# Kernel tuning notes

Measured on AMD Instinct MI355X. Metric: run time of the kernel, lower is better.

## Reference

```python
import math
import functools
import jax, jax.numpy as jnp
import numpy as np


def setup_inputs() -> dict:
    key = jax.random.key(0)
    ks = jax.random.split(key, 7)
    header = jax.random.normal(ks[0], (4, 4), dtype=jnp.float32) + 4.0 * jnp.eye(4, dtype=jnp.float32)  # well-conditioned
    vol_affine = jax.random.normal(ks[1], (4, 4), dtype=jnp.float32)
    cr = jax.random.normal(ks[2], (3,), dtype=jnp.float32)          # rotation center (mean of self.crs)
    normvec = jax.random.normal(ks[3], (3,), dtype=jnp.float32)     # mean plane normal (pre sign-align/mean)
    translation = jax.random.normal(ks[4], (3,), dtype=jnp.float32)
    angle = jax.random.normal(ks[5], (3,), dtype=jnp.float32) * 10.0  # degrees
    scaling = jax.random.normal(ks[6], (2,), dtype=jnp.float32)
    return {"header": header, "vol_affine": vol_affine, "cr": cr, "normvec": normvec,
            "translation": translation, "angle": angle, "scaling": scaling}


def _compute_affine_matrix(cr, normvec, translation, angle, scaling):
    I4 = jnp.eye(4, dtype=jnp.float32)
    nv = normvec / jnp.linalg.norm(normvec)
    norm_xy = jnp.linalg.norm(nv[:2])

    # T1 / T1inv: translate rotation center to / from origin
    T1 = I4.at[:3, 3].set(-cr)
    T1inv = I4.at[:3, 3].set(cr)

    # T2 / T2inv: rotate normal's xy-projection onto x-axis (identity if norm_xy == 0)
    zero_xy = norm_xy == 0
    safe = jnp.where(zero_xy, 1.0, norm_xy)
    a = jnp.where(zero_xy, 1.0, nv[0] / safe)
    b = jnp.where(zero_xy, 0.0, nv[1] / safe)
    T2 = I4.at[0, 0].set(a).at[0, 1].set(b).at[1, 0].set(-b).at[1, 1].set(a)
    T2inv = I4.at[0, 0].set(a).at[0, 1].set(-b).at[1, 0].set(b).at[1, 1].set(a)

    # T3 / T3inv: rotate normal onto z-axis
    T3 = I4.at[0, 0].set(nv[2]).at[0, 2].set(-norm_xy).at[2, 0].set(norm_xy).at[2, 2].set(nv[2])
    T3inv = I4.at[0, 0].set(nv[2]).at[0, 2].set(norm_xy).at[2, 0].set(-norm_xy).at[2, 2].set(nv[2])

    # T4a: anisotropic scaling (XY shared, Z separate), exp-parameterized
    sxy = jnp.exp(scaling[0] / 100.0)
    sz = jnp.exp(scaling[1] / 100.0)
    T4a = I4.at[0, 0].set(sxy).at[1, 1].set(sxy).at[2, 2].set(sz)

    # T4b1/2/3: rotations about x, y, z (angles in degrees)
    ang = angle / 180.0 * math.pi
    c, s = jnp.cos(ang), jnp.sin(ang)
    T4b1 = I4.at[1, 1].set(c[0]).at[1, 2].set(-s[0]).at[2, 1].set(s[0]).at[2, 2].set(c[0])
    T4b2 = I4.at[0, 0].set(c[1]).at[0, 2].set(s[1]).at[2, 0].set(-s[1]).at[2, 2].set(c[1])
    T4b3 = I4.at[0, 0].set(c[2]).at[0, 1].set(-s[2]).at[1, 0].set(s[2]).at[1, 1].set(c[2])

    Ttrans = I4.at[:3, 3].set(translation)

    mats = [Ttrans, T1inv, T2inv, T3inv, T4b3, T4b2, T4b1, T4a, T3, T2, T1]
    return functools.reduce(jnp.matmul, mats)


def reference(header, vol_affine, cr, normvec, translation, angle, scaling):
    ndims = 3
    T = _compute_affine_matrix(cr, normvec, translation, angle, scaling)
    new_header = T @ header                                  # [4,4]
    affine_full = jnp.linalg.inv(new_header) @ vol_affine    # [4,4]
    affine = affine_full[:ndims][None]                       # [1,3,4] (unsqueeze then [:ndims] slices batch dim of size 1)
    return affine, new_header
```

## Files before the change

kernel.cpp:

```cpp
#include <hip/hip_runtime.h>
#include <math.h>


__device__ inline void matmul4(const float* A, const float* B, float* C) {
    for (int i = 0; i < 4; ++i)
        for (int j = 0; j < 4; ++j) {
            float s = 0.0f;
            for (int k = 0; k < 4; ++k) s = fmaf(A[i*4+k], B[k*4+j], s);
            C[i*4+j] = s;
        }
}

__device__ inline void eye4(float* M) {
    for (int i = 0; i < 16; ++i) M[i] = 0.0f;
    M[0] = M[5] = M[10] = M[15] = 1.0f;
}

__global__ void affine_kernel(const float* __restrict__ header,
                              const float* __restrict__ vol_affine,
                              const float* __restrict__ cr,
                              const float* __restrict__ normvec,
                              const float* __restrict__ translation,
                              const float* __restrict__ angle,
                              const float* __restrict__ scaling,
                              float* __restrict__ out) {
    if (threadIdx.x != 0 || blockIdx.x != 0) return;

    const float PI = 3.14159265358979323846f;

    float n0 = normvec[0], n1 = normvec[1], n2 = normvec[2];
    float nn = sqrtf(fmaf(n0, n0, fmaf(n1, n1, n2 * n2)));
    float nv0 = n0 / nn, nv1 = n1 / nn, nv2 = n2 / nn;
    float norm_xy = sqrtf(fmaf(nv0, nv0, nv1 * nv1));

    bool zero_xy = (norm_xy == 0.0f);
    float safe = zero_xy ? 1.0f : norm_xy;
    float a = zero_xy ? 1.0f : nv0 / safe;
    float b = zero_xy ? 0.0f : nv1 / safe;

    float T1[16], T1inv[16], T2[16], T2inv[16], T3[16], T3inv[16];
    float T4a[16], Ttrans[16];

    eye4(T1);    T1[3]    = -cr[0]; T1[7]    = -cr[1]; T1[11]    = -cr[2];
    eye4(T1inv); T1inv[3] =  cr[0]; T1inv[7] =  cr[1]; T1inv[11] =  cr[2];

    eye4(T2);    T2[0] = a;    T2[1] = b;     T2[4] = -b;    T2[5] = a;
    eye4(T2inv); T2inv[0] = a; T2inv[1] = -b; T2inv[4] = b;  T2inv[5] = a;

    eye4(T3);    T3[0] = nv2;    T3[2] = -norm_xy;    T3[8] = norm_xy;     T3[10] = nv2;
    eye4(T3inv); T3inv[0] = nv2; T3inv[2] = norm_xy;  T3inv[8] = -norm_xy; T3inv[10] = nv2;

    float sxy = __expf(scaling[0] * 0.01f);
    float sz  = __expf(scaling[1] * 0.01f);
    eye4(T4a); T4a[0] = sxy; T4a[5] = sxy; T4a[10] = sz;

    float a0 = angle[0] * (PI / 180.0f);
    float a1 = angle[1] * (PI / 180.0f);
    float a2 = angle[2] * (PI / 180.0f);
    float s0, c0, s1, c1, s2, c2;
    __sincosf(a0, &s0, &c0);
    __sincosf(a1, &s1, &c1);
    __sincosf(a2, &s2, &c2);
    float T4b1_[16], T4b2_[16], T4b3_[16];
    eye4(T4b1_); T4b1_[5] = c0; T4b1_[6] = -s0; T4b1_[9] = s0;  T4b1_[10] = c0;
    eye4(T4b2_); T4b2_[0] = c1; T4b2_[2] = s1;  T4b2_[8] = -s1; T4b2_[10] = c1;
    eye4(T4b3_); T4b3_[0] = c2; T4b3_[1] = -s2; T4b3_[4] = s2;  T4b3_[5] = c2;

    eye4(Ttrans);
    Ttrans[3]  = translation[0];
    Ttrans[7]  = translation[1];
    Ttrans[11] = translation[2];

    float acc[16], tmp[16];
    matmul4(Ttrans, T1inv, acc);
    matmul4(acc, T2inv, tmp);
    matmul4(tmp, T3inv, acc);
    matmul4(acc, T4b3_, tmp);
    matmul4(tmp, T4b2_, acc);
    matmul4(acc, T4b1_, tmp);
    matmul4(tmp, T4a, acc);
    matmul4(acc, T3, tmp);
    matmul4(tmp, T2, acc);
    matmul4(acc, T1, tmp);

    float H[16];
    for (int i = 0; i < 16; ++i) H[i] = header[i];
    float NH[16];
    matmul4(tmp, H, NH);

    float M[16], Inv[16];
    for (int i = 0; i < 16; ++i) M[i] = NH[i];
    eye4(Inv);
    for (int col = 0; col < 4; ++col) {
        int piv = col;
        float best = fabsf(M[col * 4 + col]);
        for (int r = col + 1; r < 4; ++r) {
            float v = fabsf(M[r * 4 + col]);
            if (v > best) { best = v; piv = r; }
        }
        if (piv != col) {
            for (int j = 0; j < 4; ++j) {
                float t = M[col * 4 + j]; M[col * 4 + j] = M[piv * 4 + j]; M[piv * 4 + j] = t;
                t = Inv[col * 4 + j]; Inv[col * 4 + j] = Inv[piv * 4 + j]; Inv[piv * 4 + j] = t;
            }
        }
        float invd = 1.0f / M[col * 4 + col];
        for (int j = 0; j < 4; ++j) { M[col * 4 + j] *= invd; Inv[col * 4 + j] *= invd; }
        for (int r = 0; r < 4; ++r) {
            if (r == col) continue;
            float f = M[r * 4 + col];
            if (f != 0.0f) {
                for (int j = 0; j < 4; ++j) {
                    M[r * 4 + j]   = fmaf(-f, M[col * 4 + j],   M[r * 4 + j]);
                    Inv[r * 4 + j] = fmaf(-f, Inv[col * 4 + j], Inv[r * 4 + j]);
                }
            }
        }
    }

    float VA[16];
    for (int i = 0; i < 16; ++i) VA[i] = vol_affine[i];
    float AF[16];
    matmul4(Inv, VA, AF);

    for (int i = 0; i < 12; ++i) out[i]      = AF[i];
    for (int i = 0; i < 16; ++i) out[12 + i] = NH[i];
}

extern "C" void kernel_launch(void* const* d_in, const int* in_sizes, int n_in,
                              void* d_out, int out_size, void* d_ws, size_t ws_size,
                              hipStream_t stream) {
    const float* header      = (const float*)d_in[0];
    const float* vol_affine  = (const float*)d_in[1];
    const float* cr          = (const float*)d_in[2];
    const float* normvec     = (const float*)d_in[3];
    const float* translation = (const float*)d_in[4];
    const float* angle       = (const float*)d_in[5];
    const float* scaling     = (const float*)d_in[6];
    float* out = (float*)d_out;

    affine_kernel<<<1, 64, 0, stream>>>(header, vol_affine, cr, normvec,
                                        translation, angle, scaling, out);
}
```

Before: 9.719 us.

## Compose affine as 3x3 rotation plus translation and use closed-form 4x4 inverse

Replaces the chain of eleven 4x4 homogeneous matmuls with six 3x3 products, merging scaling into the x-rotation and folding the translate/center terms into one translation vector. Replaces pivoted Gauss-Jordan inversion with a cofactor (2x2 sub-determinant) closed-form inverse, and computes only the needed rows of the final products. This cuts serial single-thread arithmetic and branching. The closed-form inverse drops pivoting, which can change numerical accuracy for ill-conditioned headers.

```diff
diff --git a/kernel.cpp b/kernel.cpp
--- a/kernel.cpp
+++ b/kernel.cpp
@@ -2,18 +2,14 @@
 #include <math.h>
 
 
-__device__ inline void matmul4(const float* A, const float* B, float* C) {
-    for (int i = 0; i < 4; ++i)
-        for (int j = 0; j < 4; ++j) {
-            float s = 0.0f;
-            for (int k = 0; k < 4; ++k) s = fmaf(A[i*4+k], B[k*4+j], s);
-            C[i*4+j] = s;
+__device__ inline void mm3(const float* A, const float* B, float* C) {
+    for (int i = 0; i < 3; ++i)
+        for (int j = 0; j < 3; ++j) {
+            float s = A[i*3+0] * B[0*3+j];
+            s = fmaf(A[i*3+1], B[1*3+j], s);
+            s = fmaf(A[i*3+2], B[2*3+j], s);
+            C[i*3+j] = s;
         }
-}
-
-__device__ inline void eye4(float* M) {
-    for (int i = 0; i < 16; ++i) M[i] = 0.0f;
-    M[0] = M[5] = M[10] = M[15] = 1.0f;
 }
 
 __global__ void affine_kernel(const float* __restrict__ header,
@@ -31,28 +27,15 @@
     float n0 = normvec[0], n1 = normvec[1], n2 = normvec[2];
     float nn = sqrtf(fmaf(n0, n0, fmaf(n1, n1, n2 * n2)));
     float nv0 = n0 / nn, nv1 = n1 / nn, nv2 = n2 / nn;
-    float norm_xy = sqrtf(fmaf(nv0, nv0, nv1 * nv1));
+    float nxy = sqrtf(fmaf(nv0, nv0, nv1 * nv1));
 
-    bool zero_xy = (norm_xy == 0.0f);
-    float safe = zero_xy ? 1.0f : norm_xy;
+    bool zero_xy = (nxy == 0.0f);
+    float safe = zero_xy ? 1.0f : nxy;
     float a = zero_xy ? 1.0f : nv0 / safe;
     float b = zero_xy ? 0.0f : nv1 / safe;
 
-    float T1[16], T1inv[16], T2[16], T2inv[16], T3[16], T3inv[16];
-    float T4a[16], Ttrans[16];
-
-    eye4(T1);    T1[3]    = -cr[0]; T1[7]    = -cr[1]; T1[11]    = -cr[2];
-    eye4(T1inv); T1inv[3] =  cr[0]; T1inv[7] =  cr[1]; T1inv[11] =  cr[2];
-
-    eye4(T2);    T2[0] = a;    T2[1] = b;     T2[4] = -b;    T2[5] = a;
-    eye4(T2inv); T2inv[0] = a; T2inv[1] = -b; T2inv[4] = b;  T2inv[5] = a;
-
-    eye4(T3);    T3[0] = nv2;    T3[2] = -norm_xy;    T3[8] = norm_xy;     T3[10] = nv2;
-    eye4(T3inv); T3inv[0] = nv2; T3inv[2] = norm_xy;  T3inv[8] = -norm_xy; T3inv[10] = nv2;
-
     float sxy = __expf(scaling[0] * 0.01f);
     float sz  = __expf(scaling[1] * 0.01f);
-    eye4(T4a); T4a[0] = sxy; T4a[5] = sxy; T4a[10] = sz;
 
     float a0 = angle[0] * (PI / 180.0f);
     float a1 = angle[1] * (PI / 180.0f);
@@ -61,69 +44,89 @@
     __sincosf(a0, &s0, &c0);
     __sincosf(a1, &s1, &c1);
     __sincosf(a2, &s2, &c2);
-    float T4b1_[16], T4b2_[16], T4b3_[16];
-    eye4(T4b1_); T4b1_[5] = c0; T4b1_[6] = -s0; T4b1_[9] = s0;  T4b1_[10] = c0;
-    eye4(T4b2_); T4b2_[0] = c1; T4b2_[2] = s1;  T4b2_[8] = -s1; T4b2_[10] = c1;
-    eye4(T4b3_); T4b3_[0] = c2; T4b3_[1] = -s2; T4b3_[4] = s2;  T4b3_[5] = c2;
 
-    eye4(Ttrans);
-    Ttrans[3]  = translation[0];
-    Ttrans[7]  = translation[1];
-    Ttrans[11] = translation[2];
+    float T23[9]    = { a,  b, 0.0f,  -b,  a, 0.0f,  0.0f, 0.0f, 1.0f };
+    float T2inv3[9] = { a, -b, 0.0f,   b,  a, 0.0f,  0.0f, 0.0f, 1.0f };
+    float T33[9]    = { nv2, 0.0f, -nxy,  0.0f, 1.0f, 0.0f,  nxy, 0.0f, nv2 };
+    float T3inv3[9] = { nv2, 0.0f,  nxy,  0.0f, 1.0f, 0.0f, -nxy, 0.0f, nv2 };
+    float Rz[9]     = { c2, -s2, 0.0f,  s2, c2, 0.0f,  0.0f, 0.0f, 1.0f };
+    float Ry[9]     = { c1, 0.0f, s1,   0.0f, 1.0f, 0.0f,  -s1, 0.0f, c1 };
+    float RxS[9]    = { sxy, 0.0f, 0.0f,
+                        0.0f, sxy * c0, -sz * s0,
+                        0.0f, sxy * s0,  sz * c0 };
 
-    float acc[16], tmp[16];
-    matmul4(Ttrans, T1inv, acc);
-    matmul4(acc, T2inv, tmp);
-    matmul4(tmp, T3inv, acc);
-    matmul4(acc, T4b3_, tmp);
-    matmul4(tmp, T4b2_, acc);
-    matmul4(acc, T4b1_, tmp);
-    matmul4(tmp, T4a, acc);
-    matmul4(acc, T3, tmp);
-    matmul4(tmp, T2, acc);
-    matmul4(acc, T1, tmp);
+    float A1[9], A2[9], M[9];
+    mm3(T2inv3, T3inv3, A1);
+    mm3(A1, Rz, A2);
+    mm3(A2, Ry, A1);
+    mm3(A1, RxS, A2);
+    mm3(A2, T33, A1);
+    mm3(A1, T23, M);
+
+    float cr0 = cr[0], cr1 = cr[1], cr2 = cr[2];
+    float t0 = translation[0] + cr0 - (fmaf(M[0], cr0, fmaf(M[1], cr1, M[2] * cr2)));
+    float t1 = translation[1] + cr1 - (fmaf(M[3], cr0, fmaf(M[4], cr1, M[5] * cr2)));
+    float t2 = translation[2] + cr2 - (fmaf(M[6], cr0, fmaf(M[7], cr1, M[8] * cr2)));
+    float t[3] = { t0, t1, t2 };
 
     float H[16];
     for (int i = 0; i < 16; ++i) H[i] = header[i];
     float NH[16];
-    matmul4(tmp, H, NH);
+    for (int i = 0; i < 3; ++i)
+        for (int j = 0; j < 4; ++j) {
+            float s = fmaf(M[i*3+0], H[0*4+j],
+                      fmaf(M[i*3+1], H[1*4+j],
+                      fmaf(M[i*3+2], H[2*4+j],
+                           t[i] * H[3*4+j])));
+            NH[i*4+j] = s;
+        }
+    for (int j = 0; j < 4; ++j) NH[12 + j] = H[12 + j];
 
-    float M[16], Inv[16];
-    for (int i = 0; i < 16; ++i) M[i] = NH[i];
-    eye4(Inv);
-    for (int col = 0; col < 4; ++col) {
-        int piv = col;
-        float best = fabsf(M[col * 4 + col]);
-        for (int r = col + 1; r < 4; ++r) {
-            float v = fabsf(M[r * 4 + col]);
-            if (v > best) { best = v; piv = r; }
-        }
-        if (piv != col) {
-            for (int j = 0; j < 4; ++j) {
-                float t = M[col * 4 + j]; M[col * 4 + j] = M[piv * 4 + j]; M[piv * 4 + j] = t;
-                t = Inv[col * 4 + j]; Inv[col * 4 + j] = Inv[piv * 4 + j]; Inv[piv * 4 + j] = t;
-            }
-        }
-        float invd = 1.0f / M[col * 4 + col];
-        for (int j = 0; j < 4; ++j) { M[col * 4 + j] *= invd; Inv[col * 4 + j] *= invd; }
-        for (int r = 0; r < 4; ++r) {
-            if (r == col) continue;
-            float f = M[r * 4 + col];
-            if (f != 0.0f) {
-                for (int j = 0; j < 4; ++j) {
-                    M[r * 4 + j]   = fmaf(-f, M[col * 4 + j],   M[r * 4 + j]);
-                    Inv[r * 4 + j] = fmaf(-f, Inv[col * 4 + j], Inv[r * 4 + j]);
-                }
-            }
-        }
-    }
+    const float* m = NH;
+    float A_ = fmaf(m[0], m[5], -m[4] * m[1]);
+    float B_ = fmaf(m[0], m[6], -m[4] * m[2]);
+    float C_ = fmaf(m[0], m[7], -m[4] * m[3]);
+    float D_ = fmaf(m[1], m[6], -m[5] * m[2]);
+    float E_ = fmaf(m[1], m[7], -m[5] * m[3]);
+    float F_ = fmaf(m[2], m[7], -m[6] * m[3]);
+    float G_ = fmaf(m[8],  m[13], -m[12] * m[9]);
+    float Hc = fmaf(m[8],  m[14], -m[12] * m[10]);
+    float I_ = fmaf(m[8],  m[15], -m[12] * m[11]);
+    float J_ = fmaf(m[9],  m[14], -m[13] * m[10]);
+    float K_ = fmaf(m[9],  m[15], -m[13] * m[11]);
+    float L_ = fmaf(m[10], m[15], -m[14] * m[11]);
+
+    float det = A_ * L_ - B_ * K_ + C_ * J_ + D_ * I_ - E_ * Hc + F_ * G_;
+    float rd = 1.0f / det;
+
+    float Inv[16];
+    Inv[0]  = ( m[5] * L_ - m[6] * K_ + m[7] * J_) * rd;
+    Inv[1]  = (-m[1] * L_ + m[2] * K_ - m[3] * J_) * rd;
+    Inv[2]  = ( m[13] * F_ - m[14] * E_ + m[15] * D_) * rd;
+    Inv[3]  = (-m[9]  * F_ + m[10] * E_ - m[11] * D_) * rd;
+    Inv[4]  = (-m[4] * L_ + m[6] * I_ - m[7] * Hc) * rd;
+    Inv[5]  = ( m[0] * L_ - m[2] * I_ + m[3] * Hc) * rd;
+    Inv[6]  = (-m[12] * F_ + m[14] * C_ - m[15] * B_) * rd;
+    Inv[7]  = ( m[8]  * F_ - m[10] * C_ + m[11] * B_) * rd;
+    Inv[8]  = ( m[4] * K_ - m[5] * I_ + m[7] * G_) * rd;
+    Inv[9]  = (-m[0] * K_ + m[1] * I_ - m[3] * G_) * rd;
+    Inv[10] = ( m[12] * E_ - m[13] * C_ + m[15] * A_) * rd;
+    Inv[11] = (-m[8]  * E_ + m[9]  * C_ - m[11] * A_) * rd;
+    Inv[12] = (-m[4] * J_ + m[5] * Hc - m[6] * G_) * rd;
+    Inv[13] = ( m[0] * J_ - m[1] * Hc + m[2] * G_) * rd;
+    Inv[14] = (-m[12] * D_ + m[13] * B_ - m[14] * A_) * rd;
+    Inv[15] = ( m[8]  * D_ - m[9]  * B_ + m[10] * A_) * rd;
 
     float VA[16];
     for (int i = 0; i < 16; ++i) VA[i] = vol_affine[i];
-    float AF[16];
-    matmul4(Inv, VA, AF);
-
-    for (int i = 0; i < 12; ++i) out[i]      = AF[i];
+    for (int i = 0; i < 3; ++i)
+        for (int j = 0; j < 4; ++j) {
+            float s = fmaf(Inv[i*4+0], VA[0*4+j],
+                      fmaf(Inv[i*4+1], VA[1*4+j],
+                      fmaf(Inv[i*4+2], VA[2*4+j],
+                           Inv[i*4+3] * VA[3*4+j])));
+            out[i*4+j] = s;
+        }
     for (int i = 0; i < 16; ++i) out[12 + i] = NH[i];
 }
 
```

Measured after the change: 9.535 us. Within noise of the previous version (-1.9%).
